# Kernel optimization log

Measured on AMD Instinct MI355X. Metric: run time of the kernel, lower is better.

## Reference

```python
import jax, jax.numpy as jnp
import numpy as np


def _conv_nchw(x, w, strides):
    # F.conv2d with padding=0 -> VALID, NCHW / OIHW layout
    return jax.lax.conv_general_dilated(
        x, w, window_strides=tuple(strides), padding="VALID",
        dimension_numbers=("NCHW", "OIHW", "NCHW"))


def setup_inputs() -> dict:
    key = jax.random.key(0)
    kx, kw, kb = jax.random.split(key, 3)
    # scale so values span the full int8 range and all 8 bit-planes are active
    x = jax.random.normal(kx, (64, 64, 56, 56), dtype=jnp.float32) * 60.0
    weight = jax.random.normal(kw, (128, 64, 3, 3), dtype=jnp.float32) * 0.05
    bias = jax.random.normal(kb, (128,), dtype=jnp.float32)
    return {"x": x, "weight": weight, "bias": bias}


def reference(x, weight, bias):
    strides = (1, 1)
    # clamp to int8 range and cast (torch.clamp + .type(torch.int8))
    xi = jnp.clip(x, -128, 127).astype(jnp.int8)
    y = jnp.zeros((), dtype=weight.dtype)
    for i in range(8):
        # arithmetic shift on signed int8, matching torch semantics
        bit = ((xi >> i) & 1).astype(weight.dtype)
        yi = jnp.clip(_conv_nchw(bit, weight, strides), -1024, 1023)
        scale = jnp.asarray(-128.0 if i == 7 else float(2 ** i), dtype=weight.dtype)
        y = y + yi * scale
    y = y + bias.reshape(1, -1, 1, 1)
    return y
```

## Files before the change

kernel.cpp:

```cpp
#include <hip/hip_runtime.h>
#include <stdint.h>

typedef unsigned short u16;
typedef __attribute__((ext_vector_type(8))) __bf16 bf16x8;
typedef __attribute__((ext_vector_type(4))) float f32x4;
typedef __attribute__((ext_vector_type(4))) u16 u16x4;
typedef __attribute__((ext_vector_type(8))) u16 u16x8;

#define N_IMG 64
#define C_IN  64
#define HW_IN 3136
#define W_IN  56
#define C_OUT 128
#define OH    54
#define OW    54
#define SPI   2916
#define KTOT  576
#define M_TOTAL (N_IMG*SPI)
#define NWG   (M_TOTAL/128)

typedef __attribute__((address_space(3))) unsigned int lds_uint;
typedef __attribute__((address_space(1))) unsigned int gbl_uint;

__device__ __forceinline__ void load16_to_lds(const u16* g, u16* l) {
  __builtin_amdgcn_global_load_lds((const gbl_uint*)g, (lds_uint*)l, 16, 0, 0);
}

__device__ inline u16 f32_bf16_rne(float f) {
  unsigned u = __float_as_uint(f);
  u = (u + 0x7FFFu + ((u >> 16) & 1u)) >> 16;
  return (u16)u;
}

__global__ __launch_bounds__(256) void convert_xw(
    const float* __restrict__ x, const float* __restrict__ w,
    u16* __restrict__ xt, u16* __restrict__ wtT)
{
  if (blockIdx.y == N_IMG) {
    int o = blockIdx.x * 256 + threadIdx.x;
    for (; o < C_OUT * KTOT; o += 49 * 256) {
      int co = o / KTOT;
      int k  = o - co * KTOT;
      int t  = k >> 6;
      int ci = k & 63;
      wtT[o] = f32_bf16_rne(w[co * KTOT + ci * 9 + t]);
    }
    return;
  }

  __shared__ u16 tile[64][68];
  int n  = blockIdx.y;
  int s0 = blockIdx.x * 64;
  int t  = threadIdx.x;

  int r = t >> 2;
  int q = t & 3;
  const float* xp = x + (size_t)n * C_IN * HW_IN + (size_t)r * HW_IN + s0 + q * 16;
  #pragma unroll
  for (int j = 0; j < 4; j++) {
    f32x4 v = *(const f32x4*)(xp + 4 * j);
    u16x4 o4;
    #pragma unroll
    for (int e = 0; e < 4; e++) {
      float f = fminf(fmaxf(v[e], -128.f), 127.f);
      int iv = (int)f;
      o4[e] = f32_bf16_rne((float)iv);
    }
    *(u16x4*)&tile[r][q * 16 + 4 * j] = o4;
  }
  __syncthreads();

  u16* op = xt + ((size_t)n * HW_IN + s0) * C_IN;
  int g = t & 7;
  int m = t >> 3;
  #pragma unroll
  for (int k2 = 0; k2 < 2; k2++) {
    int sp = m * 2 + k2;
    u16x8 o8;
    #pragma unroll
    for (int c = 0; c < 8; c++) o8[c] = tile[g * 8 + c][sp];
    *(u16x8*)&op[(size_t)sp * C_IN + g * 8] = o8;
  }
}

__global__ __launch_bounds__(512, 4) void conv_gemm(
    const u16* __restrict__ xt, const u16* __restrict__ wtT,
    const float* __restrict__ bias, float* __restrict__ y)
{
  __shared__ u16 sP[2][128 * 64];
  __shared__ u16 sW[2][128 * 64];

  int tid  = threadIdx.x;
  int wv   = tid >> 6;
  int lane = tid & 63;
  int ln   = lane & 15;
  int q    = lane >> 4;
  int wy   = wv >> 1;
  int wx   = wv & 1;

  int orig = blockIdx.x;
  int xcd = orig & 7, j8 = orig >> 3;
  const int qq = NWG / 8, rr = NWG % 8;
  int wgid = (xcd < rr ? xcd * (qq + 1) : rr * (qq + 1) + (xcd - rr) * qq) + j8;
  int blk_sp0 = wgid * 128;

  int r8 = lane >> 3;
  int cg = lane & 7;
  int scol = (cg ^ r8) * 8;

  int pix_off[2], wt_off[2];
  #pragma unroll
  for (int j = 0; j < 2; j++) {
    int srow = wv * 16 + j * 8 + r8;
    int p   = blk_sp0 + srow;
    int img = p / SPI;  int rem = p - img * SPI;
    int oh  = rem / OW; int ow  = rem - oh * OW;
    pix_off[j] = (img * HW_IN + oh * W_IN + ow) * C_IN + scol;
    wt_off[j]  = srow * KTOT + scol;
  }

  f32x4 acc[2][4];
  #pragma unroll
  for (int mt = 0; mt < 2; mt++)
    #pragma unroll
    for (int nt = 0; nt < 4; nt++)
      acc[mt][nt] = (f32x4){0.f, 0.f, 0.f, 0.f};

  int wrow[2], prow[4];
  #pragma unroll
  for (int i = 0; i < 2; i++) wrow[i] = (wy * 32 + i * 16 + ln) * 64;
  #pragma unroll
  for (int i = 0; i < 4; i++) prow[i] = (wx * 64 + i * 16 + ln) * 64;
  int l7 = ln & 7;
  int lbase = (wv * 16) * 64;

  #pragma unroll
  for (int j = 0; j < 2; j++)
    load16_to_lds(xt + pix_off[j], &sP[0][lbase + j * 512]);
  #pragma unroll
  for (int j = 0; j < 2; j++)
    load16_to_lds(wtT + wt_off[j], &sW[0][lbase + j * 512]);

  #pragma unroll
  for (int kc = 0; kc < 9; kc++) {
    const int cur = kc & 1, nxt = cur ^ 1;

    __syncthreads();

    if (kc < 8) {
      int kn = kc + 1;
      int kh = kn / 3, kw = kn - kh * 3;
      int xoff = (kh * W_IN + kw) * C_IN;
      #pragma unroll
      for (int j = 0; j < 2; j++)
        load16_to_lds(xt + pix_off[j] + xoff, &sP[nxt][lbase + j * 512]);
      #pragma unroll
      for (int j = 0; j < 2; j++)
        load16_to_lds(wtT + wt_off[j] + kn * 64, &sW[nxt][lbase + j * 512]);
    }

    #pragma unroll
    for (int s = 0; s < 2; s++) {
      int pg = ((s * 4 + q) ^ l7) * 8;
      bf16x8 wf[2], pf[4];
      #pragma unroll
      for (int mt = 0; mt < 2; mt++)
        wf[mt] = *(const bf16x8*)(&sW[cur][0] + wrow[mt] + pg);
      #pragma unroll
      for (int nt = 0; nt < 4; nt++)
        pf[nt] = *(const bf16x8*)(&sP[cur][0] + prow[nt] + pg);
      #pragma unroll
      for (int mt = 0; mt < 2; mt++)
        #pragma unroll
        for (int nt = 0; nt < 4; nt++)
          acc[mt][nt] = __builtin_amdgcn_mfma_f32_16x16x32_bf16(
              wf[mt], pf[nt], acc[mt][nt], 0, 0, 0);
    }
  }

  #pragma unroll
  for (int nt = 0; nt < 4; nt++) {
    int p   = blk_sp0 + wx * 64 + nt * 16 + ln;
    int img = p / SPI;  int rem = p - img * SPI;
    int oh  = rem / OW; int ow  = rem - oh * OW;
    int obase = img * C_OUT * SPI + oh * OW + ow;
    #pragma unroll
    for (int mt = 0; mt < 2; mt++) {
      int co0 = wy * 32 + mt * 16 + q * 4;
      #pragma unroll
      for (int r = 0; r < 4; r++) {
        int co = co0 + r;
        y[obase + co * SPI] = acc[mt][nt][r] + bias[co];
      }
    }
  }
}

extern "C" void kernel_launch(void* const* d_in, const int* in_sizes, int n_in,
                              void* d_out, int out_size, void* d_ws, size_t ws_size,
                              hipStream_t stream) {
  const float* x    = (const float*)d_in[0];
  const float* w    = (const float*)d_in[1];
  const float* bias = (const float*)d_in[2];
  float* y = (float*)d_out;

  u16* wtT = (u16*)d_ws;
  u16* xt  = (u16*)((char*)d_ws + (size_t)C_OUT * KTOT * sizeof(u16));

  hipLaunchKernelGGL(convert_xw, dim3(HW_IN / 64, N_IMG + 1), dim3(256), 0, stream,
                     x, w, xt, wtT);
  hipLaunchKernelGGL(conv_gemm, dim3(NWG), dim3(512), 0, stream,
                     xt, wtT, bias, y);
}
```

Measured before the change: 167.9 us.

## Stage an input-row slab in LDS once and reuse it across all nine taps

The conv GEMM now tiles by image, 23 blocks of 128 output positions each. Each block loads a 256-position by 64-channel input slab into LDS once. The nine filter taps are read from that slab by shifting the row offset, instead of fetching a new pixel tile from global memory for every tap. Only the weight tile is still double-buffered per tap. This removes most repeated global and L2 reads of the transposed input. The cost is some wasted compute on the padded tail block of each image and slab reads that run past the end of the image for the last blocks.

```diff
diff --git a/kernel.cpp b/kernel.cpp
--- a/kernel.cpp
+++ b/kernel.cpp
@@ -16,8 +16,9 @@
 #define OW    54
 #define SPI   2916
 #define KTOT  576
-#define M_TOTAL (N_IMG*SPI)
-#define NWG   (M_TOTAL/128)
+#define NBPI  23
+#define NWG   (N_IMG*NBPI)
+#define SLAB_POS 256
 
 typedef __attribute__((address_space(3))) unsigned int lds_uint;
 typedef __attribute__((address_space(1))) unsigned int gbl_uint;
@@ -87,7 +88,7 @@
     const u16* __restrict__ xt, const u16* __restrict__ wtT,
     const float* __restrict__ bias, float* __restrict__ y)
 {
-  __shared__ u16 sP[2][128 * 64];
+  __shared__ u16 slab[SLAB_POS * 64];
   __shared__ u16 sW[2][128 * 64];
 
   int tid  = threadIdx.x;
@@ -97,26 +98,31 @@
   int q    = lane >> 4;
   int wy   = wv >> 1;
   int wx   = wv & 1;
-
-  int orig = blockIdx.x;
-  int xcd = orig & 7, j8 = orig >> 3;
-  const int qq = NWG / 8, rr = NWG % 8;
-  int wgid = (xcd < rr ? xcd * (qq + 1) : rr * (qq + 1) + (xcd - rr) * qq) + j8;
-  int blk_sp0 = wgid * 128;
+  int l7   = ln & 7;
+
+  int b  = blockIdx.x;
+  int wg = (b & 7) * (NWG / 8) + (b >> 3);
+  int img = wg / NBPI;
+  int cb  = wg - img * NBPI;
+  int r0  = cb * 128;
+  int ibase = r0 + 2 * (r0 / OW);
+
+  const u16* xg = xt + ((size_t)img * HW_IN + ibase) * C_IN;
 
   int r8 = lane >> 3;
   int cg = lane & 7;
   int scol = (cg ^ r8) * 8;
-
-  int pix_off[2], wt_off[2];
-  #pragma unroll
-  for (int j = 0; j < 2; j++) {
-    int srow = wv * 16 + j * 8 + r8;
-    int p   = blk_sp0 + srow;
-    int img = p / SPI;  int rem = p - img * SPI;
-    int oh  = rem / OW; int ow  = rem - oh * OW;
-    pix_off[j] = (img * HW_IN + oh * W_IN + ow) * C_IN + scol;
-    wt_off[j]  = srow * KTOT + scol;
+  int wt_off[2];
+  #pragma unroll
+  for (int j = 0; j < 2; j++)
+    wt_off[j] = (wv * 16 + j * 8 + r8) * KTOT + scol;
+
+  int slab_src[4];
+  #pragma unroll
+  for (int j = 0; j < 4; j++) {
+    int slot = j * 512 + tid;
+    int row  = slot >> 3, cgc = slot & 7;
+    slab_src[j] = row * 64 + ((cgc ^ (row & 7)) * 8);
   }
 
   f32x4 acc[2][4];
@@ -126,49 +132,51 @@
     for (int nt = 0; nt < 4; nt++)
       acc[mt][nt] = (f32x4){0.f, 0.f, 0.f, 0.f};
 
-  int wrow[2], prow[4];
+  int prel[4], rbase[4];
+  #pragma unroll
+  for (int nt = 0; nt < 4; nt++) {
+    int pr = r0 + wx * 64 + nt * 16 + ln;
+    prel[nt]  = pr;
+    rbase[nt] = pr + 2 * (pr / OW) - ibase;
+  }
+  int wrow[2];
   #pragma unroll
   for (int i = 0; i < 2; i++) wrow[i] = (wy * 32 + i * 16 + ln) * 64;
-  #pragma unroll
-  for (int i = 0; i < 4; i++) prow[i] = (wx * 64 + i * 16 + ln) * 64;
-  int l7 = ln & 7;
-  int lbase = (wv * 16) * 64;
-
+
+  #pragma unroll
+  for (int j = 0; j < 4; j++)
+    load16_to_lds(xg + slab_src[j], slab + (size_t)(j * 512 + wv * 64) * 8);
   #pragma unroll
   for (int j = 0; j < 2; j++)
-    load16_to_lds(xt + pix_off[j], &sP[0][lbase + j * 512]);
-  #pragma unroll
-  for (int j = 0; j < 2; j++)
-    load16_to_lds(wtT + wt_off[j], &sW[0][lbase + j * 512]);
+    load16_to_lds(wtT + wt_off[j], &sW[0][(wv * 16 + j * 8) * 64]);
 
   #pragma unroll
   for (int kc = 0; kc < 9; kc++) {
     const int cur = kc & 1, nxt = cur ^ 1;
+    const int kh = kc / 3, kw = kc - kh * 3;
+    const int koff = kh * W_IN + kw;
 
     __syncthreads();
 
     if (kc < 8) {
-      int kn = kc + 1;
-      int kh = kn / 3, kw = kn - kh * 3;
-      int xoff = (kh * W_IN + kw) * C_IN;
       #pragma unroll
       for (int j = 0; j < 2; j++)
-        load16_to_lds(xt + pix_off[j] + xoff, &sP[nxt][lbase + j * 512]);
-      #pragma unroll
-      for (int j = 0; j < 2; j++)
-        load16_to_lds(wtT + wt_off[j] + kn * 64, &sW[nxt][lbase + j * 512]);
+        load16_to_lds(wtT + wt_off[j] + (kc + 1) * 64, &sW[nxt][(wv * 16 + j * 8) * 64]);
     }
 
     #pragma unroll
     for (int s = 0; s < 2; s++) {
-      int pg = ((s * 4 + q) ^ l7) * 8;
+      int g = s * 4 + q;
+      int pgW = (g ^ l7) * 8;
       bf16x8 wf[2], pf[4];
       #pragma unroll
       for (int mt = 0; mt < 2; mt++)
-        wf[mt] = *(const bf16x8*)(&sW[cur][0] + wrow[mt] + pg);
-      #pragma unroll
-      for (int nt = 0; nt < 4; nt++)
-        pf[nt] = *(const bf16x8*)(&sP[cur][0] + prow[nt] + pg);
+        wf[mt] = *(const bf16x8*)(&sW[cur][0] + wrow[mt] + pgW);
+      #pragma unroll
+      for (int nt = 0; nt < 4; nt++) {
+        int rb = rbase[nt] + koff;
+        pf[nt] = *(const bf16x8*)(slab + rb * 64 + ((g ^ (rb & 7)) * 8));
+      }
       #pragma unroll
       for (int mt = 0; mt < 2; mt++)
         #pragma unroll
@@ -178,19 +186,17 @@
     }
   }
 
+  size_t obase0 = (size_t)img * C_OUT * SPI;
   #pragma unroll
   for (int nt = 0; nt < 4; nt++) {
-    int p   = blk_sp0 + wx * 64 + nt * 16 + ln;
-    int img = p / SPI;  int rem = p - img * SPI;
-    int oh  = rem / OW; int ow  = rem - oh * OW;
-    int obase = img * C_OUT * SPI + oh * OW + ow;
-    #pragma unroll
-    for (int mt = 0; mt < 2; mt++) {
-      int co0 = wy * 32 + mt * 16 + q * 4;
-      #pragma unroll
-      for (int r = 0; r < 4; r++) {
-        int co = co0 + r;
-        y[obase + co * SPI] = acc[mt][nt][r] + bias[co];
+    int pr = prel[nt];
+    if (pr < SPI) {
+      #pragma unroll
+      for (int mt = 0; mt < 2; mt++) {
+        int co0 = wy * 32 + mt * 16 + q * 4;
+        #pragma unroll
+        for (int r = 0; r < 4; r++)
+          y[obase0 + (size_t)(co0 + r) * SPI + pr] = acc[mt][nt][r] + bias[co0 + r];
       }
     }
   }
```

After: 170.6 us. Within noise of the previous version (+1.6%).
